# Kernel tuning notes

Hardware: AMD Instinct MI355X
Metric: run time of the kernel (lower is better)

## Reference

```python
import jax, jax.numpy as jnp
import numpy as np

N = 100000   # num 'note' nodes
E = 1000000  # edges per relation
R = 3        # relation types (onset, consecutive, during)
IN = 128
OUT = 64
NEG_SLOPE = 0.2  # GATConv default leaky_relu slope


def setup_inputs() -> dict:
    key = jax.random.key(0)
    ks = jax.random.split(key, 13)
    x = jax.random.normal(ks[0], (N, IN), jnp.float32)
    ei0 = jax.random.randint(ks[1], (2, E), 0, N)
    ei1 = jax.random.randint(ks[2], (2, E), 0, N)
    ei2 = jax.random.randint(ks[3], (2, E), 0, N)
    s1 = 1.0 / np.sqrt(IN)
    s2 = 1.0 / np.sqrt(OUT)
    W1 = jax.random.normal(ks[4], (R, IN, OUT), jnp.float32) * s1
    a_src1 = jax.random.normal(ks[5], (R, OUT), jnp.float32) * s2
    a_dst1 = jax.random.normal(ks[6], (R, OUT), jnp.float32) * s2
    b1 = jnp.zeros((R, OUT), jnp.float32)
    W2 = jax.random.normal(ks[7], (R, OUT, OUT), jnp.float32) * s2
    a_src2 = jax.random.normal(ks[8], (R, OUT), jnp.float32) * s2
    a_dst2 = jax.random.normal(ks[9], (R, OUT), jnp.float32) * s2
    b2 = jnp.zeros((R, OUT), jnp.float32)
    return dict(x=x, ei0=ei0, ei1=ei1, ei2=ei2,
                W1=W1, a_src1=a_src1, a_dst1=a_dst1, b1=b1,
                W2=W2, a_src2=a_src2, a_dst2=a_dst2, b2=b2)


def _gat_relation(x, ei, W, a_src, a_dst, b):
    # single-head GATConv for one relation (aggr='sum' over edges)
    h = x @ W                              # [N, OUT]
    src, dst = ei[0], ei[1]
    al_src = h @ a_src                     # [N]
    al_dst = h @ a_dst                     # [N]
    e = jax.nn.leaky_relu(al_src[src] + al_dst[dst], NEG_SLOPE)  # [E]
    # segment softmax over incoming edges per destination node
    m = jax.ops.segment_max(e, dst, num_segments=N)              # [N]
    num = jnp.exp(e - m[dst])                                    # [E]
    den = jax.ops.segment_sum(num, dst, num_segments=N)          # [N]
    coef = num / den[dst]                                        # [E]
    msg = coef[:, None] * h[src]                                 # [E, OUT]
    return jax.ops.segment_sum(msg, dst, num_segments=N) + b     # [N, OUT]


def _hetero_layer(x, eis, W, a_src, a_dst, b):
    # to_hetero: per-relation GATConv, then mean across relations
    outs = [_gat_relation(x, eis[r], W[r], a_src[r], a_dst[r], b[r]) for r in range(R)]
    return jnp.mean(jnp.stack(outs, 0), 0)


def _l2norm(v):
    # F.normalize(v, dim=-1), eps=1e-12
    n = jnp.linalg.norm(v, axis=-1, keepdims=True)
    return v / jnp.maximum(n, 1e-12)


def reference(x, ei0, ei1, ei2, W1, a_src1, a_dst1, b1, W2, a_src2, a_dst2, b2):
    eis = [ei0, ei1, ei2]
    h = _hetero_layer(x, eis, W1, a_src1, a_dst1, b1)
    h = jax.nn.relu(_l2norm(h))  # dropout is identity in eval mode
    out = _hetero_layer(h, eis, W2, a_src2, a_dst2, b2)
    return out  # x_dict['note']
```

## Files before the change

kernel.cpp:

```cpp
#include <hip/hip_runtime.h>
#include <hip/hip_bf16.h>
#include <hip/hip_fp16.h>
#include <math.h>

constexpr int NN = 100000;
constexpr int EE = 1000000;
constexpr int RRR = 3;
constexpr int DIN = 128;
constexpr int DOUT = 64;
constexpr float SLOPE = 0.2f;
constexpr int NR = RRR * NN;
constexpr int BSEG = 256;
constexpr int NBUCK = (NR + BSEG - 1) / BSEG;
constexpr int BCAP = 4096;
constexpr int CHUNK_E = 8192;
constexpr int NCH_PER_R = (EE + CHUNK_E - 1) / CHUNK_E;
constexpr int NCH = RRR * NCH_PER_R;
constexpr int MT = NBUCK * NCH;
constexpr int SCAN_CHUNK = 1024;
constexpr int NSCB = (MT + SCAN_CHUNK - 1) / SCAN_CHUNK;

using f16x8 = __attribute__((ext_vector_type(8))) _Float16;
using f32x4 = __attribute__((ext_vector_type(4))) float;

template<int CTRL>
__device__ __forceinline__ float dppf(float v) {
    return __int_as_float(__builtin_amdgcn_update_dpp(
        __float_as_int(v), __float_as_int(v), CTRL, 0xf, 0xf, false));
}
__device__ __forceinline__ float dpp_allred_add16(float v) {
    v += dppf<0xB1>(v);
    v += dppf<0x4E>(v);
    v += dppf<0x141>(v);
    v += dppf<0x140>(v);
    return v;
}

__global__ __launch_bounds__(256) void pack_W(
    const float* __restrict__ W1, const float* __restrict__ W2,
    const float* __restrict__ b1, const float* __restrict__ b2,
    __half* __restrict__ Wp1, __half* __restrict__ Wp2,
    float* __restrict__ bs1, float* __restrict__ bs2)
{
    int r = blockIdx.x;
    for (int i = threadIdx.x; i < 4 * 4 * 512; i += 256) {
        int j = i & 7, lane = (i >> 3) & 63, nt = (i >> 9) & 3, ks = i >> 11;
        int k = ks * 32 + (lane >> 4) * 8 + j, c = nt * 16 + (lane & 15);
        Wp1[((size_t)r * 16 + ks * 4 + nt) * 512 + lane * 8 + j] = __float2half(W1[(r * DIN + k) * 64 + c]);
    }
    for (int i = threadIdx.x; i < 2 * 4 * 512; i += 256) {
        int j = i & 7, lane = (i >> 3) & 63, nt = (i >> 9) & 3, ks = i >> 11;
        int k = ks * 32 + (lane >> 4) * 8 + j, c = nt * 16 + (lane & 15);
        Wp2[((size_t)r * 8 + ks * 4 + nt) * 512 + lane * 8 + j] = __float2half(W2[(r * DOUT + k) * 64 + c]);
    }
    if (r == 0) {
        for (int c = threadIdx.x; c < 64; c += 256) {
            bs1[c] = (b1[c] + b1[64 + c] + b1[128 + c]) * (1.f / 3.f);
            bs2[c] = (b2[c] + b2[64 + c] + b2[128 + c]) * (1.f / 3.f);
        }
    }
}

template<int K, typename AT>
__global__ __launch_bounds__(256) void gemm_mfma2(
    const AT* __restrict__ xin,
    const __half* __restrict__ Wp,
    const float* __restrict__ asrc, const float* __restrict__ adst,
    __half* __restrict__ h,
    float* __restrict__ als, float* __restrict__ ald)
{
    constexpr int KS = K / 32;
    __shared__ float outb[64 * 65];
    const int t = threadIdx.x;
    const int lane = t & 63;
    const int w = t >> 6;
    const int row0 = blockIdx.x * 64;

    const int kgrp = lane >> 4;
    const int l15 = lane & 15;
    int arow = row0 + w * 16 + l15; if (arow >= NN) arow = NN - 1;

    f16x8 a[KS];
    if constexpr (sizeof(AT) == 2) {
        const __half* ab = (const __half*)xin + (size_t)arow * K + kgrp * 8;
#pragma unroll
        for (int ks = 0; ks < KS; ++ks) a[ks] = *(const f16x8*)(ab + ks * 32);
    } else {
        const float* ab = (const float*)xin + (size_t)arow * K + kgrp * 8;
#pragma unroll
        for (int ks = 0; ks < KS; ++ks) {
            float4 lo = *(const float4*)(ab + ks * 32);
            float4 hi = *(const float4*)(ab + ks * 32 + 4);
            union { f16x8 v; __half2 p[4]; } u;
            u.p[0] = __floats2half2_rn(lo.x, lo.y);
            u.p[1] = __floats2half2_rn(lo.z, lo.w);
            u.p[2] = __floats2half2_rn(hi.x, hi.y);
            u.p[3] = __floats2half2_rn(hi.z, hi.w);
            a[ks] = u.v;
        }
    }

    const int nrows = (NN - row0 < 64) ? (NN - row0) : 64;

#pragma unroll
    for (int r = 0; r < RRR; ++r) {
        const __half* wbase = Wp + ((size_t)r * KS * 4) * 512 + lane * 8;
        f32x4 acc[4] = {};
#pragma unroll
        for (int ks = 0; ks < KS; ++ks) {
#pragma unroll
            for (int nt = 0; nt < 4; ++nt) {
                f16x8 b = *(const f16x8*)(wbase + (size_t)(ks * 4 + nt) * 512);
                acc[nt] = __builtin_amdgcn_mfma_f32_16x16x32_f16(a[ks], b, acc[nt], 0, 0, 0);
            }
        }

        {
            float ps[4] = {0.f, 0.f, 0.f, 0.f}, pd[4] = {0.f, 0.f, 0.f, 0.f};
#pragma unroll
            for (int nt = 0; nt < 4; ++nt) {
                int c = l15 + 16 * nt;
                float a_ = asrc[r * 64 + c], d_ = adst[r * 64 + c];
#pragma unroll
                for (int i = 0; i < 4; ++i) {
                    ps[i] = fmaf(acc[nt][i], a_, ps[i]);
                    pd[i] = fmaf(acc[nt][i], d_, pd[i]);
                }
            }
#pragma unroll
            for (int o = 8; o; o >>= 1) {
#pragma unroll
                for (int i = 0; i < 4; ++i) {
                    ps[i] += __shfl_xor(ps[i], o);
                    pd[i] += __shfl_xor(pd[i], o);
                }
            }
            if (l15 == 0) {
#pragma unroll
                for (int i = 0; i < 4; ++i) {
                    int row = row0 + w * 16 + kgrp * 4 + i;
                    if (row < NN) { als[r * NN + row] = ps[i]; ald[r * NN + row] = pd[i]; }
                }
            }
        }

#pragma unroll
        for (int nt = 0; nt < 4; ++nt)
#pragma unroll
            for (int i = 0; i < 4; ++i)
                outb[(w * 16 + kgrp * 4 + i) * 65 + l15 + 16 * nt] = acc[nt][i];
        __syncthreads();

        __half2* h2 = (__half2*)(h + ((size_t)r * NN + row0) * 64);
        for (int idx = t; idx < nrows * 32; idx += 256) {
            int row = idx >> 5, cc = idx & 31;
            h2[row * 32 + cc] = __floats2half2_rn(outb[row * 65 + cc * 2], outb[row * 65 + cc * 2 + 1]);
        }
        __syncthreads();
    }
}


__global__ __launch_bounds__(256) void chunk_hist(
    const int* __restrict__ ei0, const int* __restrict__ ei1, const int* __restrict__ ei2,
    unsigned* __restrict__ M)
{
    __shared__ unsigned hist[NBUCK];
    const int r = blockIdx.y, bx = blockIdx.x;
    const int* ei = (r == 0) ? ei0 : ((r == 1) ? ei1 : ei2);
    const int t = threadIdx.x;
    for (int i = t; i < NBUCK; i += 256) hist[i] = 0;
    __syncthreads();
    const int e0 = bx * CHUNK_E;
    const int e1 = (e0 + CHUNK_E < EE) ? e0 + CHUNK_E : EE;
    for (int e = e0 + t; e < e1; e += 256) {
        int idx = r * NN + ei[EE + e];
        atomicAdd(&hist[idx >> 8], 1u);
    }
    __syncthreads();
    const int c = r * NCH_PER_R + bx;
    for (int i = t; i < NBUCK; i += 256) M[(size_t)i * NCH + c] = hist[i];
}

__global__ __launch_bounds__(256) void scan_block(unsigned* __restrict__ data, unsigned* __restrict__ bsum)
{
    __shared__ unsigned tsum[256];
    const int base = blockIdx.x * SCAN_CHUNK;
    const int t = threadIdx.x;
    const int i0 = base + t * 4;
    unsigned v[4];
#pragma unroll
    for (int k = 0; k < 4; ++k) v[k] = (i0 + k < MT) ? data[i0 + k] : 0u;
    unsigned run = 0;
#pragma unroll
    for (int k = 0; k < 4; ++k) { unsigned x = v[k]; v[k] = run; run += x; }
    tsum[t] = run;
    __syncthreads();
    unsigned val = run;
    for (int d = 1; d < 256; d <<= 1) {
        unsigned add = (t >= d) ? tsum[t - d] : 0u;
        __syncthreads();
        val += add;
        tsum[t] = val;
        __syncthreads();
    }
    unsigned texcl = val - run;
    if (t == 255) bsum[blockIdx.x] = val;
#pragma unroll
    for (int k = 0; k < 4; ++k)
        if (i0 + k < MT) data[i0 + k] = texcl + v[k];
}

__global__ __launch_bounds__(256) void scan_bsums(unsigned* __restrict__ bsum)
{
    __shared__ unsigned s[NSCB];
    int t = threadIdx.x;
    for (int i = t; i < NSCB; i += 256) s[i] = bsum[i];
    __syncthreads();
    if (t == 0) {
        unsigned run = 0;
        for (int i = 0; i < NSCB; ++i) { unsigned x = s[i]; s[i] = run; run += x; }
    }
    __syncthreads();
    for (int i = t; i < NSCB; i += 256) bsum[i] = s[i];
}

__global__ __launch_bounds__(256) void add_off(unsigned* __restrict__ data, const unsigned* __restrict__ bsum)
{
    int i = blockIdx.x * 256 + threadIdx.x;
    if (i >= MT) return;
    data[i] += bsum[i / SCAN_CHUNK];
}

__global__ __launch_bounds__(256) void chunk_scatter(
    const int* __restrict__ ei0, const int* __restrict__ ei1, const int* __restrict__ ei2,
    const unsigned* __restrict__ Ms, unsigned* __restrict__ packed)
{
    __shared__ unsigned cur[NBUCK];
    const int r = blockIdx.y, bx = blockIdx.x;
    const int* ei = (r == 0) ? ei0 : ((r == 1) ? ei1 : ei2);
    const int t = threadIdx.x;
    const int c = r * NCH_PER_R + bx;
    for (int i = t; i < NBUCK; i += 256) cur[i] = Ms[(size_t)i * NCH + c];
    __syncthreads();
    const int e0 = bx * CHUNK_E;
    const int e1 = (e0 + CHUNK_E < EE) ? e0 + CHUNK_E : EE;
    for (int e = e0 + t; e < e1; e += 256) {
        int src = ei[e];
        int idx = r * NN + ei[EE + e];
        unsigned pos = atomicAdd(&cur[idx >> 8], 1u);
        packed[pos] = (unsigned)src | ((unsigned)(idx & 255) << 24);
    }
}

__global__ __launch_bounds__(256) void bucket_build(
    unsigned* __restrict__ packed,
    const unsigned* __restrict__ Ms,
    unsigned* __restrict__ off)
{
    __shared__ unsigned sp[BCAP];
    __shared__ unsigned ssrc[BCAP];
    __shared__ unsigned scnt[BSEG];
    __shared__ unsigned scur[BSEG];
    __shared__ unsigned tsum[BSEG];
    const int b = blockIdx.x;
    const int t = threadIdx.x;
    const unsigned base = Ms[(size_t)b * NCH];
    const unsigned next = (b + 1 < NBUCK) ? Ms[(size_t)(b + 1) * NCH] : (unsigned)((size_t)RRR * EE);
    int cnt = (int)(next - base);
    if (cnt > BCAP) cnt = BCAP;
    for (int i = t; i < cnt; i += 256) sp[i] = packed[base + i];
    scnt[t] = 0;
    __syncthreads();
    for (int i = t; i < cnt; i += 256) atomicAdd(&scnt[sp[i] >> 24], 1u);
    __syncthreads();
    unsigned v = scnt[t];
    tsum[t] = v;
    __syncthreads();
    unsigned val = v;
    for (int d = 1; d < 256; d <<= 1) {
        unsigned add = (t >= d) ? tsum[t - d] : 0u;
        __syncthreads();
        val += add;
        tsum[t] = val;
        __syncthreads();
    }
    unsigned excl = val - v;
    scur[t] = excl;
    const int segs = (NR - b * BSEG < BSEG) ? (NR - b * BSEG) : BSEG;
    if (t < segs) off[b * BSEG + t] = base + excl;
    __syncthreads();
    for (int i = t; i < cnt; i += 256) {
        unsigned p = sp[i];
        unsigned pos = atomicAdd(&scur[p >> 24], 1u);
        ssrc[pos] = p & 0x00FFFFFFu;
    }
    __syncthreads();
    for (int i = t; i < cnt; i += 256) packed[base + i] = ssrc[i];
}

template<bool L1>
__global__ __launch_bounds__(256) void aggregate10(
    const int* __restrict__ csr_src, const unsigned* __restrict__ off,
    const __half* __restrict__ h,
    const float* __restrict__ als, const float* __restrict__ ald,
    const float* __restrict__ bsum3,
    float* __restrict__ outp,
    __half* __restrict__ outH)
{
    __shared__ float sbuf[4][64];
    const int wid = threadIdx.x >> 6;
    const int lane = threadIdx.x & 63;
    const int nh = lane >> 5;
    const int l31 = lane & 31;
    const int sub = l31 >> 4;
    const int fc = l31 & 15;
    const int node = blockIdx.x * 8 + wid * 2 + nh;

    unsigned start[RRR]; int cnt[RRR]; float aldv[RRR];
    int maxcnt = 0;
#pragma unroll
    for (int r = 0; r < RRR; ++r) {
        int idx = r * NN + node;
        unsigned s = off[idx];
        unsigned e = (idx == NR - 1) ? (unsigned)((size_t)RRR * EE) : off[idx + 1];
        start[r] = s; cnt[r] = (int)(e - s); aldv[r] = ald[idx];
        if (cnt[r] > maxcnt) maxcnt = cnt[r];
    }

    float4 total = make_float4(0.f, 0.f, 0.f, 0.f);

    if (__all(maxcnt <= 32)) {
        int srcv[RRR]; float p[RRR], den[RRR];
#pragma unroll
        for (int r = 0; r < RRR; ++r) {
            bool act = l31 < cnt[r];
            int s_ = act ? csr_src[start[r] + l31] : 0;
            srcv[r] = s_;
            float sv = act ? (als[r * NN + s_] + aldv[r]) : -3.0e38f;
            float lr = (sv > 0.f) ? sv : SLOPE * sv;
            lr = fminf(lr, 60.f);
            p[r] = __expf(lr);
            den[r] = dpp_allred_add16(p[r]);
        }
#pragma unroll
        for (int r = 0; r < RRR; ++r) den[r] += __shfl_xor(den[r], 16);
#pragma unroll
        for (int r = 0; r < RRR; ++r) {
            float inv = (cnt[r] > 0) ? 1.f / den[r] : 0.f;
            p[r] *= inv;
        }

        float4 acc = make_float4(0.f, 0.f, 0.f, 0.f);
#pragma unroll
        for (int r = 0; r < RRR; ++r) {
            const __half* hr = h + (size_t)r * NN * DOUT;
            const int nq = (cnt[r] + 7) >> 3;
            for (int q = 0; q < nq; ++q) {
                const int base = q * 8;
                float pl[4]; int sl[4];
#pragma unroll
                for (int l = 0; l < 4; ++l) {
                    int e = base + l * 2 + sub;
                    pl[l] = __shfl(p[r], nh * 32 + e);
                    sl[l] = __shfl(srcv[r], nh * 32 + e);
                }
                uint2 rl[4];
#pragma unroll
                for (int l = 0; l < 4; ++l)
                    rl[l] = *(const uint2*)(hr + (size_t)sl[l] * DOUT + fc * 4);
#pragma unroll
                for (int l = 0; l < 4; ++l) {
                    float2 f01 = __half22float2(*(const __half2*)&rl[l].x);
                    float2 f23 = __half22float2(*(const __half2*)&rl[l].y);
                    acc.x = fmaf(pl[l], f01.x, acc.x);
                    acc.y = fmaf(pl[l], f01.y, acc.y);
                    acc.z = fmaf(pl[l], f23.x, acc.z);
                    acc.w = fmaf(pl[l], f23.y, acc.w);
                }
            }
        }
        acc.x += __shfl_xor(acc.x, 16); acc.y += __shfl_xor(acc.y, 16);
        acc.z += __shfl_xor(acc.z, 16); acc.w += __shfl_xor(acc.w, 16);
        total = acc;
    } else {
        for (int nn = 0; nn < 2; ++nn) {
            int node2 = blockIdx.x * 8 + wid * 2 + nn;
            float totalS = 0.f;
#pragma unroll
            for (int r = 0; r < RRR; ++r) {
                int idx = r * NN + node2;
                unsigned s2 = off[idx];
                unsigned e2 = (idx == NR - 1) ? (unsigned)((size_t)RRR * EE) : off[idx + 1];
                int c2 = (int)(e2 - s2);
                if (c2 <= 0) continue;
                float aldv2 = ald[idx];
                const __half* hr = h + (size_t)r * NN * DOUT;
                const float* alsr = als + (size_t)r * NN;
                float m = -3.4e38f, den = 0.f, accv = 0.f;
                for (int t0 = 0; t0 < c2; t0 += 64) {
                    int j = t0 + lane;
                    bool act = (j < c2);
                    int src = 0;
                    float lrv = -3.4e38f;
                    if (act) {
                        src = csr_src[s2 + j];
                        float sv = alsr[src] + aldv2;
                        lrv = (sv > 0.f) ? sv : SLOPE * sv;
                    }
                    float mt = lrv;
#pragma unroll
                    for (int o = 32; o; o >>= 1) mt = fmaxf(mt, __shfl_xor(mt, o));
                    float mnew = fmaxf(m, mt);
                    float scale = __expf(m - mnew);
                    den *= scale; accv *= scale; m = mnew;
                    float pp = act ? __expf(lrv - m) : 0.f;
                    float ps = pp;
#pragma unroll
                    for (int o = 32; o; o >>= 1) ps += __shfl_xor(ps, o);
                    den += ps;
                    int tcnt = c2 - t0; if (tcnt > 64) tcnt = 64;
                    for (int j2 = 0; j2 < tcnt; ++j2) {
                        int sj = __builtin_amdgcn_readlane(src, j2);
                        float pj = __int_as_float(__builtin_amdgcn_readlane(__float_as_int(pp), j2));
                        accv = fmaf(pj, __half2float(hr[(size_t)sj * DOUT + lane]), accv);
                    }
                }
                totalS += accv / den;
            }
            sbuf[wid][lane] = totalS;
            __builtin_amdgcn_s_waitcnt(0);
            if (nh == nn) total = *(const float4*)&sbuf[wid][fc * 4];
            __builtin_amdgcn_s_waitcnt(0);
        }
    }

    float4 bb = *(const float4*)(bsum3 + fc * 4);
    float4 v;
    v.x = fmaf(total.x, 1.f / 3.f, bb.x);
    v.y = fmaf(total.y, 1.f / 3.f, bb.y);
    v.z = fmaf(total.z, 1.f / 3.f, bb.z);
    v.w = fmaf(total.w, 1.f / 3.f, bb.w);
    if (L1) {
        float ss = v.x * v.x + v.y * v.y + v.z * v.z + v.w * v.w;
        ss = dpp_allred_add16(ss);
        float di = 1.f / fmaxf(sqrtf(ss), 1e-12f);
        v.x = fmaxf(v.x * di, 0.f);
        v.y = fmaxf(v.y * di, 0.f);
        v.z = fmaxf(v.z * di, 0.f);
        v.w = fmaxf(v.w * di, 0.f);
        if (sub == 0) {
            __half2* o2 = (__half2*)(outH + (size_t)node * DOUT + fc * 4);
            o2[0] = __floats2half2_rn(v.x, v.y);
            o2[1] = __floats2half2_rn(v.z, v.w);
        }
    } else {
        if (sub == 0) *(float4*)(outp + (size_t)node * DOUT + fc * 4) = v;
    }
}

extern "C" void kernel_launch(void* const* d_in, const int* in_sizes, int n_in,
                              void* d_out, int out_size, void* d_ws, size_t ws_size,
                              hipStream_t stream) {
    const float* x   = (const float*)d_in[0];
    const int* ei0   = (const int*)d_in[1];
    const int* ei1   = (const int*)d_in[2];
    const int* ei2   = (const int*)d_in[3];
    const float* W1  = (const float*)d_in[4];
    const float* as1 = (const float*)d_in[5];
    const float* ad1 = (const float*)d_in[6];
    const float* b1  = (const float*)d_in[7];
    const float* W2  = (const float*)d_in[8];
    const float* as2 = (const float*)d_in[9];
    const float* ad2 = (const float*)d_in[10];
    const float* b2  = (const float*)d_in[11];
    float* out = (float*)d_out;

    float* ws = (float*)d_ws;
    size_t off_u = 0;
    __half* h       = (__half*)(ws + off_u); off_u += (size_t)RRR * NN * DOUT / 2;
    float* als      = ws + off_u; off_u += (size_t)RRR * NN;
    float* ald      = ws + off_u; off_u += (size_t)RRR * NN;
    unsigned* packed= (unsigned*)(ws + off_u); off_u += (size_t)RRR * EE;
    unsigned* off   = (unsigned*)(ws + off_u); off_u += NR;
    __half* hmid_h  = (__half*)(ws + off_u); off_u += (size_t)NN * DOUT / 2;
    __half* Wp1     = (__half*)(ws + off_u); off_u += (3 * 16 * 512) / 2;
    __half* Wp2     = (__half*)(ws + off_u); off_u += (3 * 8 * 512) / 2;
    float* bs1      = ws + off_u; off_u += 64;
    float* bs2      = ws + off_u; off_u += 64;
    unsigned* M     = (unsigned*)(ws + off_u); off_u += MT;
    unsigned* bsum  = (unsigned*)(ws + off_u); off_u += NSCB + 8;

    dim3 blk(256);
    int gG = (NN + 63) / 64;
    dim3 gC(NCH_PER_R, RRR);
    int gA = (NN + 7) / 8;

    chunk_hist<<<gC, blk, 0, stream>>>(ei0, ei1, ei2, M);
    scan_block<<<NSCB, blk, 0, stream>>>(M, bsum);
    scan_bsums<<<1, blk, 0, stream>>>(bsum);
    add_off<<<(MT + 255) / 256, blk, 0, stream>>>(M, bsum);
    chunk_scatter<<<gC, blk, 0, stream>>>(ei0, ei1, ei2, M, packed);
    bucket_build<<<NBUCK, blk, 0, stream>>>(packed, M, off);
    const int* csr_src = (const int*)packed;

    pack_W<<<3, blk, 0, stream>>>(W1, W2, b1, b2, Wp1, Wp2, bs1, bs2);

    gemm_mfma2<DIN, float><<<gG, blk, 0, stream>>>(x, Wp1, as1, ad1, h, als, ald);
    aggregate10<true><<<gA, blk, 0, stream>>>(csr_src, off, h, als, ald, bs1, out, hmid_h);

    gemm_mfma2<DOUT, __half><<<gG, blk, 0, stream>>>(hmid_h, Wp2, as2, ad2, h, als, ald);
    aggregate10<false><<<gA, blk, 0, stream>>>(csr_src, off, h, als, ald, bs2, out, hmid_h);
}
```

Baseline: 263.5 us.

## Fuse layer-1 GEMM with edge histogram; merge scan steps; halve edge chunk

Layer-1 GEMM blocks and the per-chunk destination histogram blocks now run in one combined launch, dispatched on block index, so the two independent stages overlap. The single-block serial scan of block sums and the separate add-offset kernel are replaced by one kernel in which each block reduces its own prefix of block sums. The edge chunk size is halved, giving more histogram and scatter blocks but a larger count matrix to scan. The aim is fewer launches and better occupancy in the preprocessing phase. The cost is redundant prefix work per block and more scan traffic.

```diff
diff --git a/kernel.cpp b/kernel.cpp
--- a/kernel.cpp
+++ b/kernel.cpp
@@ -13,12 +13,13 @@
 constexpr int BSEG = 256;
 constexpr int NBUCK = (NR + BSEG - 1) / BSEG;
 constexpr int BCAP = 4096;
-constexpr int CHUNK_E = 8192;
+constexpr int CHUNK_E = 4096;
 constexpr int NCH_PER_R = (EE + CHUNK_E - 1) / CHUNK_E;
 constexpr int NCH = RRR * NCH_PER_R;
 constexpr int MT = NBUCK * NCH;
 constexpr int SCAN_CHUNK = 1024;
 constexpr int NSCB = (MT + SCAN_CHUNK - 1) / SCAN_CHUNK;
+constexpr int GEMM_BLKS = (NN + 63) / 64;
 
 using f16x8 = __attribute__((ext_vector_type(8))) _Float16;
 using f32x4 = __attribute__((ext_vector_type(4))) float;
@@ -62,7 +63,8 @@
 }
 
 template<int K, typename AT>
-__global__ __launch_bounds__(256) void gemm_mfma2(
+__device__ __forceinline__ void gemm_body(
+    int gbid,
     const AT* __restrict__ xin,
     const __half* __restrict__ Wp,
     const float* __restrict__ asrc, const float* __restrict__ adst,
@@ -74,7 +76,7 @@
     const int t = threadIdx.x;
     const int lane = t & 63;
     const int w = t >> 6;
-    const int row0 = blockIdx.x * 64;
+    const int row0 = gbid * 64;
 
     const int kgrp = lane >> 4;
     const int l15 = lane & 15;
@@ -160,13 +162,13 @@
     }
 }
 
-
-__global__ __launch_bounds__(256) void chunk_hist(
+__device__ __forceinline__ void hist_body(
+    int hb,
     const int* __restrict__ ei0, const int* __restrict__ ei1, const int* __restrict__ ei2,
     unsigned* __restrict__ M)
 {
     __shared__ unsigned hist[NBUCK];
-    const int r = blockIdx.y, bx = blockIdx.x;
+    const int r = hb / NCH_PER_R, bx = hb % NCH_PER_R;
     const int* ei = (r == 0) ? ei0 : ((r == 1) ? ei1 : ei2);
     const int t = threadIdx.x;
     for (int i = t; i < NBUCK; i += 256) hist[i] = 0;
@@ -182,6 +184,28 @@
     for (int i = t; i < NBUCK; i += 256) M[(size_t)i * NCH + c] = hist[i];
 }
 
+__global__ __launch_bounds__(256) void fused_prep(
+    const float* __restrict__ x, const __half* __restrict__ Wp1,
+    const float* __restrict__ as1, const float* __restrict__ ad1,
+    __half* __restrict__ h, float* __restrict__ als, float* __restrict__ ald,
+    const int* __restrict__ ei0, const int* __restrict__ ei1, const int* __restrict__ ei2,
+    unsigned* __restrict__ M)
+{
+    if ((int)blockIdx.x < GEMM_BLKS)
+        gemm_body<DIN, float>(blockIdx.x, x, Wp1, as1, ad1, h, als, ald);
+    else
+        hist_body(blockIdx.x - GEMM_BLKS, ei0, ei1, ei2, M);
+}
+
+template<int K, typename AT>
+__global__ __launch_bounds__(256) void gemm_mfma2(
+    const AT* __restrict__ xin, const __half* __restrict__ Wp,
+    const float* __restrict__ asrc, const float* __restrict__ adst,
+    __half* __restrict__ h, float* __restrict__ als, float* __restrict__ ald)
+{
+    gemm_body<K, AT>(blockIdx.x, xin, Wp, asrc, adst, h, als, ald);
+}
+
 __global__ __launch_bounds__(256) void scan_block(unsigned* __restrict__ data, unsigned* __restrict__ bsum)
 {
     __shared__ unsigned tsum[256];
@@ -211,25 +235,23 @@
         if (i0 + k < MT) data[i0 + k] = texcl + v[k];
 }
 
-__global__ __launch_bounds__(256) void scan_bsums(unsigned* __restrict__ bsum)
-{
-    __shared__ unsigned s[NSCB];
-    int t = threadIdx.x;
-    for (int i = t; i < NSCB; i += 256) s[i] = bsum[i];
-    __syncthreads();
-    if (t == 0) {
-        unsigned run = 0;
-        for (int i = 0; i < NSCB; ++i) { unsigned x = s[i]; s[i] = run; run += x; }
-    }
-    __syncthreads();
-    for (int i = t; i < NSCB; i += 256) bsum[i] = s[i];
-}
-
-__global__ __launch_bounds__(256) void add_off(unsigned* __restrict__ data, const unsigned* __restrict__ bsum)
-{
-    int i = blockIdx.x * 256 + threadIdx.x;
-    if (i >= MT) return;
-    data[i] += bsum[i / SCAN_CHUNK];
+__global__ __launch_bounds__(256) void scan_add(unsigned* __restrict__ data, const unsigned* __restrict__ bsum)
+{
+    __shared__ unsigned red[256];
+    const int b = blockIdx.x, t = threadIdx.x;
+    unsigned part = 0;
+    for (int j = t; j < b; j += 256) part += bsum[j];
+    red[t] = part;
+    __syncthreads();
+    for (int s = 128; s; s >>= 1) {
+        if (t < s) red[t] += red[t + s];
+        __syncthreads();
+    }
+    unsigned P = red[0];
+    const int i0 = b * SCAN_CHUNK + t * 4;
+#pragma unroll
+    for (int k = 0; k < 4; ++k)
+        if (i0 + k < MT) data[i0 + k] += P;
 }
 
 __global__ __launch_bounds__(256) void chunk_scatter(
@@ -492,23 +514,22 @@
     unsigned* bsum  = (unsigned*)(ws + off_u); off_u += NSCB + 8;
 
     dim3 blk(256);
-    int gG = (NN + 63) / 64;
     dim3 gC(NCH_PER_R, RRR);
     int gA = (NN + 7) / 8;
 
-    chunk_hist<<<gC, blk, 0, stream>>>(ei0, ei1, ei2, M);
+    pack_W<<<3, blk, 0, stream>>>(W1, W2, b1, b2, Wp1, Wp2, bs1, bs2);
+
+    fused_prep<<<GEMM_BLKS + NCH, blk, 0, stream>>>(
+        x, Wp1, as1, ad1, h, als, ald, ei0, ei1, ei2, M);
+
     scan_block<<<NSCB, blk, 0, stream>>>(M, bsum);
-    scan_bsums<<<1, blk, 0, stream>>>(bsum);
-    add_off<<<(MT + 255) / 256, blk, 0, stream>>>(M, bsum);
+    scan_add<<<NSCB, blk, 0, stream>>>(M, bsum);
     chunk_scatter<<<gC, blk, 0, stream>>>(ei0, ei1, ei2, M, packed);
     bucket_build<<<NBUCK, blk, 0, stream>>>(packed, M, off);
     const int* csr_src = (const int*)packed;
 
-    pack_W<<<3, blk, 0, stream>>>(W1, W2, b1, b2, Wp1, Wp2, bs1, bs2);
-
-    gemm_mfma2<DIN, float><<<gG, blk, 0, stream>>>(x, Wp1, as1, ad1, h, als, ald);
     aggregate10<true><<<gA, blk, 0, stream>>>(csr_src, off, h, als, ald, bs1, out, hmid_h);
 
-    gemm_mfma2<DOUT, __half><<<gG, blk, 0, stream>>>(hmid_h, Wp2, as2, ad2, h, als, ald);
+    gemm_mfma2<DOUT, __half><<<GEMM_BLKS, blk, 0, stream>>>(hmid_h, Wp2, as2, ad2, h, als, ald);
     aggregate10<false><<<gA, blk, 0, stream>>>(csr_src, off, h, als, ald, bs2, out, hmid_h);
 }
```

New measurement: 256.8 us, median of 2. -2.5%, faster.
